# Kernel tuning notes

Hardware: AMD Instinct MI355X
Metric: run time of the kernel (lower is better)

## Reference

```python
import jax, jax.numpy as jnp
import numpy as np

EMBED_DIM = 1024
NUM_HEADS = 16
HEAD_DIM = EMBED_DIM // NUM_HEADS
ROPE_BASE = 10000.0


def rotate_half(x):
    d = x.shape[-1] // 2
    x1, x2 = x[..., :d], x[..., d:]
    return jnp.concatenate((-x2, x1), axis=-1)


def setup_inputs() -> dict:
    key = jax.random.key(0)
    k_x, k_wqkv, k_bqkv, k_wo, k_bo = jax.random.split(key, 5)
    C = EMBED_DIM
    x = jax.random.normal(k_x, (4, 2048, C), dtype=jnp.float32)
    s = 1.0 / np.sqrt(C)
    W_qkv = jax.random.uniform(k_wqkv, (C, 3 * C), minval=-s, maxval=s, dtype=jnp.float32)
    b_qkv = jax.random.uniform(k_bqkv, (3 * C,), minval=-s, maxval=s, dtype=jnp.float32)
    W_out = jax.random.uniform(k_wo, (C, C), minval=-s, maxval=s, dtype=jnp.float32)
    b_out = jax.random.uniform(k_bo, (C,), minval=-s, maxval=s, dtype=jnp.float32)
    return {"x": x, "W_qkv": W_qkv, "b_qkv": b_qkv, "W_out": W_out, "b_out": b_out}


def reference(x, W_qkv, b_qkv, W_out, b_out):
    B, T, C = x.shape
    H, Dh = NUM_HEADS, HEAD_DIM
    # fused QKV projection: [B,T,3C] -> [3,B,H,T,Dh]
    qkv = (x @ W_qkv + b_qkv).reshape(B, T, 3, H, Dh).transpose(2, 0, 3, 1, 4)
    q, k, v = qkv[0], qkv[1], qkv[2]
    # rotary embedding: freqs [T, Dh/2] -> emb [T, Dh]
    inv_freq = 1.0 / (ROPE_BASE ** (jnp.arange(0, Dh, 2, dtype=jnp.float32) / Dh))
    freqs = jnp.arange(T, dtype=jnp.float32)[:, None] * inv_freq[None, :]
    emb = jnp.concatenate((freqs, freqs), axis=-1)  # [T, Dh], broadcasts over B,H
    cos, sin = jnp.cos(emb), jnp.sin(emb)
    q = q * cos + rotate_half(q) * sin
    k = k * cos + rotate_half(k) * sin
    # full (non-causal) attention, manual softmax
    scale = 1.0 / np.sqrt(Dh)
    attn = jax.nn.softmax(jnp.einsum("bhqd,bhkd->bhqk", q, k) * scale, axis=-1)
    out = jnp.einsum("bhqk,bhkd->bhqd", attn, v)  # [B,H,T,Dh]
    out = out.transpose(0, 2, 1, 3).reshape(B, T, C)
    return out @ W_out + b_out
```

## Files before the change

kernel.cpp:

```cpp
#include <hip/hip_runtime.h>
#include <math.h>

#define T_SEQ 2048
#define CDIM  1024
#define NH    16
#define DHD   64
#define BATCH 4
#define MROWS (BATCH * T_SEQ)
#define BHN   (BATCH * NH)

typedef _Float16 f16;
typedef __attribute__((ext_vector_type(8))) _Float16 f16x8;
typedef __attribute__((ext_vector_type(4))) _Float16 f16x4;
typedef __attribute__((ext_vector_type(4))) float f32x4;

__device__ __forceinline__ void gl_lds16(const f16* g, f16* l) {
    __builtin_amdgcn_global_load_lds(
        (const __attribute__((address_space(1))) void*)(g),
        (__attribute__((address_space(3))) void*)(l),
        16, 0, 0);
}

__global__ void rope_tables_kernel(float* __restrict__ ctab, float* __restrict__ stab)
{
    int idx = blockIdx.x * 256 + threadIdx.x;
    int t = idx >> 5, i = idx & 31;
    double inv = pow(10000.0, -(double)(2 * i) / 64.0);
    double a = (double)t * inv;
    ctab[idx] = (float)cos(a);
    stab[idx] = (float)sin(a);
}

__global__ __launch_bounds__(256) void xcvt_kernel(
    const float* __restrict__ X, f16* __restrict__ Xf)
{
    int idx = blockIdx.x * 256 + threadIdx.x;
    const float4* src = (const float4*)X + (size_t)idx * 2;
    float4 a = src[0], b = src[1];
    f16x8 o;
    o[0] = (f16)a.x; o[1] = (f16)a.y; o[2] = (f16)a.z; o[3] = (f16)a.w;
    o[4] = (f16)b.x; o[5] = (f16)b.y; o[6] = (f16)b.z; o[7] = (f16)b.w;
    *((f16x8*)Xf + idx) = o;
}

__global__ __launch_bounds__(64) void wcvt_kernel(
    const float* __restrict__ W, f16* __restrict__ Wt, int N)
{
    int lane = threadIdx.x;
    int k0 = blockIdx.x * 8;
    int n = blockIdx.y * 64 + lane;
    f16x8 o;
#pragma unroll
    for (int j = 0; j < 8; j++) o[j] = (f16)W[(size_t)(k0 + j) * N + n];
    *(f16x8*)(Wt + (size_t)n * CDIM + k0) = o;
}

#define GEMM_MAINLOOP(Aimg, Bimg, M0, N0)                                         \
    __shared__ f16 As[128][32], Bs[128][32];                                      \
    const int tid = threadIdx.x, wave = tid >> 6, lane = tid & 63;                \
    const int l16 = lane & 15, quad = lane >> 4;                                  \
    const int wm = wave >> 1, wn = wave & 1;                                      \
    f32x4 acc[4][4];                                                              \
    _Pragma("unroll") for (int i = 0; i < 4; i++)                                 \
        _Pragma("unroll") for (int j = 0; j < 4; j++)                             \
            acc[i][j] = (f32x4){0.f, 0.f, 0.f, 0.f};                              \
    const f16* sbase = (wave < 2) ? (Aimg) : (Bimg);                              \
    f16* lbase = ((wave < 2) ? &As[0][0] : &Bs[0][0]) + (wave & 1) * 2048;        \
    const size_t srow0 = ((wave < 2) ? (size_t)(M0) : (size_t)(N0)) + (wave & 1) * 64; \
    const int srow = lane >> 2, schunk = (lane & 3) << 3;                         \
    for (int k0 = 0; k0 < CDIM; k0 += 32) {                                       \
        _Pragma("unroll") for (int it = 0; it < 4; it++)                          \
            gl_lds16(sbase + (srow0 + it * 16 + srow) * CDIM + k0 + schunk,       \
                     lbase + it * 512);                                           \
        __syncthreads();                                                          \
        f16x8 fa[4], fb[4];                                                       \
        _Pragma("unroll") for (int mi = 0; mi < 4; mi++)                          \
            fa[mi] = *(const f16x8*)&As[wm * 64 + mi * 16 + l16][quad * 8];       \
        _Pragma("unroll") for (int ni = 0; ni < 4; ni++)                          \
            fb[ni] = *(const f16x8*)&Bs[wn * 64 + ni * 16 + l16][quad * 8];       \
        _Pragma("unroll") for (int mi = 0; mi < 4; mi++)                          \
            _Pragma("unroll") for (int ni = 0; ni < 4; ni++)                      \
                acc[mi][ni] = __builtin_amdgcn_mfma_f32_16x16x32_f16(             \
                    fa[mi], fb[ni], acc[mi][ni], 0, 0, 0);                        \
        __syncthreads();                                                          \
    }

__global__ __launch_bounds__(256) void qkv_gemm_kernel(
    const f16* __restrict__ Xf, const f16* __restrict__ Wt,
    const float* __restrict__ bias,
    const float* __restrict__ ctab, const float* __restrict__ stab,
    f16* __restrict__ qf, f16* __restrict__ kf, f16* __restrict__ vf)
{
    const int m0 = blockIdx.x * 128;
    const int n0 = blockIdx.y * 128;
    GEMM_MAINLOOP(Xf, Wt, m0, n0)

    const int ncol0 = n0 + wn * 64;
    const int w = ncol0 >> 10;
    const int h = (ncol0 >> 6) & 15;
    const int b = m0 >> 11;
    const int trow0 = (m0 & 2047) + wm * 64 + quad * 4;
    float bia[4];
#pragma unroll
    for (int ni = 0; ni < 4; ni++) bia[ni] = bias[ncol0 + ni * 16 + l16];

    if (w < 2) {
        f16* oq = w ? kf : qf;
        const float sc = w ? 1.0f : 0.125f;
#pragma unroll
        for (int mi = 0; mi < 4; mi++) {
#pragma unroll
            for (int i = 0; i < 4; i++) {
                int t = trow0 + mi * 16 + i;
                size_t rowoff = ((size_t)(b * NH + h) * T_SEQ + t) * DHD;
#pragma unroll
                for (int np = 0; np < 2; np++) {
                    int d = np * 16 + l16;
                    float v0 = acc[mi][np][i] + bia[np];
                    float v1 = acc[mi][np + 2][i] + bia[np + 2];
                    float c = ctab[(t << 5) + d];
                    float s = stab[(t << 5) + d];
                    oq[rowoff + d]      = (f16)((v0 * c - v1 * s) * sc);
                    oq[rowoff + d + 32] = (f16)((v1 * c + v0 * s) * sc);
                }
            }
        }
    } else {
#pragma unroll
        for (int mi = 0; mi < 4; mi++) {
#pragma unroll
            for (int i = 0; i < 4; i++) {
                int t = trow0 + mi * 16 + i;
                size_t rowoff = ((size_t)(b * NH + h) * T_SEQ + t) * DHD;
#pragma unroll
                for (int ni = 0; ni < 4; ni++)
                    vf[rowoff + ni * 16 + l16] = (f16)(acc[mi][ni][i] + bia[ni]);
            }
        }
    }
}

__global__ __launch_bounds__(256) void vt_kernel(
    const f16* __restrict__ vf, f16* __restrict__ vt)
{
    __shared__ f16 Ls[64][72];
    const int tid = threadIdx.x;
    const int tb = blockIdx.x;
    const int bh = blockIdx.y;
#pragma unroll
    for (int p = 0; p < 2; p++) {
        int idx = tid + p * 256;
        int r = idx >> 3, c8 = (idx & 7) << 3;
        *(f16x8*)&Ls[r][c8] =
            *(const f16x8*)(vf + ((size_t)bh * T_SEQ + tb * 64 + r) * DHD + c8);
    }
    __syncthreads();
#pragma unroll
    for (int p = 0; p < 2; p++) {
        int idx = tid + p * 256;
        int d = idx >> 3, t8 = (idx & 7) << 3;
        f16x8 o;
#pragma unroll
        for (int j = 0; j < 8; j++) o[j] = Ls[t8 + j][d];
        *(f16x8*)(vt + ((size_t)bh * DHD + d) * T_SEQ + (size_t)tb * 64 + t8) = o;
    }
}

__global__ __launch_bounds__(256, 2) void attn_kernel(
    const f16* __restrict__ qf, const f16* __restrict__ kf,
    const f16* __restrict__ vt, f16* __restrict__ ab)
{
    __shared__ f16 Kb[2][64][72];
    __shared__ f16 Vb[2][64][72];
    __shared__ f16 Pb[4][64][40];
    __shared__ float Lb[4][64];

    const int tid  = threadIdx.x;
    const int wave = tid >> 6, lane = tid & 63;
    const int l16  = lane & 15, quad = lane >> 4;
    const int qt = blockIdx.x;
    const int bh = blockIdx.y;
    const int q0 = qt * 256 + wave * 64;

    const f16* kbase = kf + (size_t)bh * T_SEQ * DHD;
    const f16* vbase = vt + (size_t)bh * DHD * T_SEQ;

    f16x8 qfr[4][2];
#pragma unroll
    for (int qs = 0; qs < 4; qs++) {
        const f16* qrow = qf + ((size_t)bh * T_SEQ + q0 + qs * 16 + l16) * DHD;
        qfr[qs][0] = *(const f16x8*)(qrow + quad * 8);
        qfr[qs][1] = *(const f16x8*)(qrow + 32 + quad * 8);
    }

    f32x4 o[4][4];
#pragma unroll
    for (int qs = 0; qs < 4; qs++)
#pragma unroll
        for (int dt = 0; dt < 4; dt++) o[qs][dt] = (f32x4){0.f, 0.f, 0.f, 0.f};
    float lp[4] = {0.f, 0.f, 0.f, 0.f};

    const int srow = tid >> 3;
    const int scol = (tid & 7) << 3;

    f16x8 kreg[2], vreg[2];
#pragma unroll
    for (int r = 0; r < 2; r++) {
        kreg[r] = *(const f16x8*)(kbase + (size_t)(srow + r * 32) * DHD + scol);
        vreg[r] = *(const f16x8*)(vbase + (size_t)(srow + r * 32) * T_SEQ + scol);
    }
#pragma unroll
    for (int r = 0; r < 2; r++) {
        *(f16x8*)&Kb[0][srow + r * 32][scol] = kreg[r];
        *(f16x8*)&Vb[0][srow + r * 32][scol] = vreg[r];
    }
    __syncthreads();

    for (int kt = 0; kt < 32; kt++) {
        const int buf = kt & 1;
        if (kt < 31) {
#pragma unroll
            for (int r = 0; r < 2; r++) {
                kreg[r] = *(const f16x8*)(kbase + (size_t)((kt + 1) * 64 + srow + r * 32) * DHD + scol);
                vreg[r] = *(const f16x8*)(vbase + (size_t)(srow + r * 32) * T_SEQ + (kt + 1) * 64 + scol);
            }
        }

#pragma unroll
        for (int half = 0; half < 2; half++) {
            f32x4 sc[2][4];
#pragma unroll
            for (int k2 = 0; k2 < 2; k2++)
#pragma unroll
                for (int qs = 0; qs < 4; qs++) sc[k2][qs] = (f32x4){0.f, 0.f, 0.f, 0.f};
#pragma unroll
            for (int k2 = 0; k2 < 2; k2++) {
                const int keyt = half * 2 + k2;
#pragma unroll
                for (int ks = 0; ks < 2; ks++) {
                    f16x8 kfr = *(const f16x8*)&Kb[buf][keyt * 16 + l16][ks * 32 + quad * 8];
#pragma unroll
                    for (int qs = 0; qs < 4; qs++)
                        sc[k2][qs] = __builtin_amdgcn_mfma_f32_16x16x32_f16(
                            kfr, qfr[qs][ks], sc[k2][qs], 0, 0, 0);
                }
            }
#pragma unroll
            for (int k2 = 0; k2 < 2; k2++) {
#pragma unroll
                for (int qs = 0; qs < 4; qs++) {
                    f16x4 pv;
#pragma unroll
                    for (int i = 0; i < 4; i++) {
                        float p = __expf(sc[k2][qs][i]);
                        lp[qs] += p;
                        pv[i] = (f16)p;
                    }
                    *(f16x4*)&Pb[wave][qs * 16 + l16][k2 * 16 + quad * 4] = pv;
                }
            }
            f16x8 pfr[4];
#pragma unroll
            for (int qs = 0; qs < 4; qs++)
                pfr[qs] = *(const f16x8*)&Pb[wave][qs * 16 + l16][quad * 8];
#pragma unroll
            for (int dt = 0; dt < 4; dt++) {
                f16x8 vfr = *(const f16x8*)&Vb[buf][dt * 16 + l16][half * 32 + quad * 8];
#pragma unroll
                for (int qs = 0; qs < 4; qs++)
                    o[qs][dt] = __builtin_amdgcn_mfma_f32_16x16x32_f16(
                        pfr[qs], vfr, o[qs][dt], 0, 0, 0);
            }
        }

        if (kt < 31) {
#pragma unroll
            for (int r = 0; r < 2; r++) {
                *(f16x8*)&Kb[buf ^ 1][srow + r * 32][scol] = kreg[r];
                *(f16x8*)&Vb[buf ^ 1][srow + r * 32][scol] = vreg[r];
            }
        }
        __syncthreads();
    }

#pragma unroll
    for (int qs = 0; qs < 4; qs++) {
        float l = lp[qs];
        l += __shfl_xor(l, 16);
        l += __shfl_xor(l, 32);
        Lb[wave][qs * 16 + l16] = 1.f / l;
    }

    const int b = bh >> 4, h = bh & 15;
#pragma unroll
    for (int qs = 0; qs < 4; qs++) {
        f32x4 iv = *(const f32x4*)&Lb[wave][qs * 16 + quad * 4];
#pragma unroll
        for (int i = 0; i < 4; i++) {
            int m = b * T_SEQ + qt * 256 + wave * 64 + qs * 16 + quad * 4 + i;
#pragma unroll
            for (int dt = 0; dt < 4; dt++)
                ab[(size_t)m * CDIM + h * 64 + dt * 16 + l16] = (f16)(o[qs][dt][i] * iv[i]);
        }
    }
}

__global__ __launch_bounds__(256) void out_gemm_kernel(
    const f16* __restrict__ Ab, const f16* __restrict__ Wt,
    const float* __restrict__ bias, float* __restrict__ out)
{
    const int m0 = blockIdx.x * 128;
    const int n0 = blockIdx.y * 128;
    GEMM_MAINLOOP(Ab, Wt, m0, n0)

    const int ncol0 = n0 + wn * 64;
    float bia[4];
#pragma unroll
    for (int ni = 0; ni < 4; ni++) bia[ni] = bias[ncol0 + ni * 16 + l16];
#pragma unroll
    for (int mi = 0; mi < 4; mi++) {
#pragma unroll
        for (int i = 0; i < 4; i++) {
            int m = m0 + wm * 64 + mi * 16 + quad * 4 + i;
#pragma unroll
            for (int ni = 0; ni < 4; ni++)
                out[(size_t)m * CDIM + ncol0 + ni * 16 + l16] = acc[mi][ni][i] + bia[ni];
        }
    }
}

extern "C" void kernel_launch(void* const* d_in, const int* in_sizes, int n_in,
                              void* d_out, int out_size, void* d_ws, size_t ws_size,
                              hipStream_t stream)
{
    const float* x    = (const float*)d_in[0];
    const float* Wqkv = (const float*)d_in[1];
    const float* bqkv = (const float*)d_in[2];
    const float* Wout = (const float*)d_in[3];
    const float* bout = (const float*)d_in[4];
    float* out = (float*)d_out;

    const size_t XSZ  = (size_t)MROWS * CDIM;
    const size_t WQSZ = (size_t)3072 * CDIM;
    const size_t WOSZ = (size_t)CDIM * CDIM;
    const size_t QSZ  = (size_t)BHN * T_SEQ * DHD;

    char* p = (char*)d_ws;
    f16* Xf  = (f16*)p; p += XSZ * 2;
    f16* Wqt = (f16*)p; p += WQSZ * 2;
    f16* Wot = (f16*)p; p += WOSZ * 2;
    f16* qf  = (f16*)p; p += QSZ * 2;
    f16* kf  = (f16*)p; p += QSZ * 2;
    f16* vf  = (f16*)p; p += QSZ * 2;
    f16* vtb = (f16*)p; p += QSZ * 2;
    f16* ab  = (f16*)p; p += QSZ * 2;
    float* ctab = (float*)p; p += T_SEQ * 32 * 4;
    float* stab = (float*)p; p += T_SEQ * 32 * 4;

    rope_tables_kernel<<<256, 256, 0, stream>>>(ctab, stab);
    xcvt_kernel<<<(int)(XSZ / 8 / 256), 256, 0, stream>>>(x, Xf);
    wcvt_kernel<<<dim3(128, 48), 64, 0, stream>>>(Wqkv, Wqt, 3072);
    wcvt_kernel<<<dim3(128, 16), 64, 0, stream>>>(Wout, Wot, 1024);
    qkv_gemm_kernel<<<dim3(64, 24), 256, 0, stream>>>(
        Xf, Wqt, bqkv, ctab, stab, qf, kf, vf);
    vt_kernel<<<dim3(32, BHN), 256, 0, stream>>>(vf, vtb);
    attn_kernel<<<dim3(8, BHN), 256, 0, stream>>>(qf, kf, vtb, ab);
    out_gemm_kernel<<<dim3(64, 8), 256, 0, stream>>>(ab, Wot, bout, out);
}
```

Baseline: 307.1 us.

## Single-buffer attention LDS, raise occupancy, fold log2e into Q for exp2

```diff
diff --git a/kernel.cpp b/kernel.cpp
--- a/kernel.cpp
+++ b/kernel.cpp
@@ -106,7 +106,7 @@
 
     if (w < 2) {
         f16* oq = w ? kf : qf;
-        const float sc = w ? 1.0f : 0.125f;
+        const float sc = w ? 1.0f : 0.125f * 1.44269504088896f;
 #pragma unroll
         for (int mi = 0; mi < 4; mi++) {
 #pragma unroll
@@ -166,20 +166,21 @@
     }
 }
 
-__global__ __launch_bounds__(256, 2) void attn_kernel(
+__global__ __launch_bounds__(256, 3) void attn_kernel(
     const f16* __restrict__ qf, const f16* __restrict__ kf,
     const f16* __restrict__ vt, f16* __restrict__ ab)
 {
-    __shared__ f16 Kb[2][64][72];
-    __shared__ f16 Vb[2][64][72];
-    __shared__ f16 Pb[4][64][40];
+    __shared__ f16 Kb[64][68];
+    __shared__ f16 Vb[64][68];
+    __shared__ f16 Pb[4][64][36];
     __shared__ float Lb[4][64];
 
     const int tid  = threadIdx.x;
     const int wave = tid >> 6, lane = tid & 63;
     const int l16  = lane & 15, quad = lane >> 4;
-    const int qt = blockIdx.x;
-    const int bh = blockIdx.y;
+    const int bid = blockIdx.x;
+    const int bh = bid & 63;
+    const int qt = bid >> 6;
     const int q0 = qt * 256 + wave * 64;
 
     const f16* kbase = kf + (size_t)bh * T_SEQ * DHD;
@@ -204,27 +205,23 @@
     const int scol = (tid & 7) << 3;
 
     f16x8 kreg[2], vreg[2];
-#pragma unroll
-    for (int r = 0; r < 2; r++) {
-        kreg[r] = *(const f16x8*)(kbase + (size_t)(srow + r * 32) * DHD + scol);
-        vreg[r] = *(const f16x8*)(vbase + (size_t)(srow + r * 32) * T_SEQ + scol);
-    }
-#pragma unroll
-    for (int r = 0; r < 2; r++) {
-        *(f16x8*)&Kb[0][srow + r * 32][scol] = kreg[r];
-        *(f16x8*)&Vb[0][srow + r * 32][scol] = vreg[r];
-    }
+#define PREFETCH(KT)                                                              \
+    _Pragma("unroll") for (int r = 0; r < 2; r++) {                               \
+        kreg[r] = *(const f16x8*)(kbase + (size_t)((KT) * 64 + srow + r * 32) * DHD + scol); \
+        vreg[r] = *(const f16x8*)(vbase + (size_t)(srow + r * 32) * T_SEQ + (KT) * 64 + scol); \
+    }
+#define COMMIT()                                                                  \
+    _Pragma("unroll") for (int r = 0; r < 2; r++) {                               \
+        *(f16x8*)&Kb[srow + r * 32][scol] = kreg[r];                              \
+        *(f16x8*)&Vb[srow + r * 32][scol] = vreg[r];                              \
+    }
+
+    PREFETCH(0)
+    COMMIT()
     __syncthreads();
 
     for (int kt = 0; kt < 32; kt++) {
-        const int buf = kt & 1;
-        if (kt < 31) {
-#pragma unroll
-            for (int r = 0; r < 2; r++) {
-                kreg[r] = *(const f16x8*)(kbase + (size_t)((kt + 1) * 64 + srow + r * 32) * DHD + scol);
-                vreg[r] = *(const f16x8*)(vbase + (size_t)(srow + r * 32) * T_SEQ + (kt + 1) * 64 + scol);
-            }
-        }
+        if (kt < 31) { PREFETCH(kt + 1) }
 
 #pragma unroll
         for (int half = 0; half < 2; half++) {
@@ -238,7 +235,7 @@
                 const int keyt = half * 2 + k2;
 #pragma unroll
                 for (int ks = 0; ks < 2; ks++) {
-                    f16x8 kfr = *(const f16x8*)&Kb[buf][keyt * 16 + l16][ks * 32 + quad * 8];
+                    f16x8 kfr = *(const f16x8*)&Kb[keyt * 16 + l16][ks * 32 + quad * 8];
 #pragma unroll
                     for (int qs = 0; qs < 4; qs++)
                         sc[k2][qs] = __builtin_amdgcn_mfma_f32_16x16x32_f16(
@@ -249,13 +246,14 @@
             for (int k2 = 0; k2 < 2; k2++) {
 #pragma unroll
                 for (int qs = 0; qs < 4; qs++) {
+                    float p0 = exp2f(sc[k2][qs][0]);
+                    float p1 = exp2f(sc[k2][qs][1]);
+                    float p2 = exp2f(sc[k2][qs][2]);
+                    float p3 = exp2f(sc[k2][qs][3]);
+                    lp[qs] += (p0 + p1) + (p2 + p3);
                     f16x4 pv;
-#pragma unroll
-                    for (int i = 0; i < 4; i++) {
-                        float p = __expf(sc[k2][qs][i]);
-                        lp[qs] += p;
-                        pv[i] = (f16)p;
-                    }
+                    pv[0] = (f16)p0; pv[1] = (f16)p1;
+                    pv[2] = (f16)p2; pv[3] = (f16)p3;
                     *(f16x4*)&Pb[wave][qs * 16 + l16][k2 * 16 + quad * 4] = pv;
                 }
             }
@@ -265,7 +263,7 @@
                 pfr[qs] = *(const f16x8*)&Pb[wave][qs * 16 + l16][quad * 8];
 #pragma unroll
             for (int dt = 0; dt < 4; dt++) {
-                f16x8 vfr = *(const f16x8*)&Vb[buf][dt * 16 + l16][half * 32 + quad * 8];
+                f16x8 vfr = *(const f16x8*)&Vb[dt * 16 + l16][half * 32 + quad * 8];
 #pragma unroll
                 for (int qs = 0; qs < 4; qs++)
                     o[qs][dt] = __builtin_amdgcn_mfma_f32_16x16x32_f16(
@@ -273,15 +271,12 @@
             }
         }
 
-        if (kt < 31) {
-#pragma unroll
-            for (int r = 0; r < 2; r++) {
-                *(f16x8*)&Kb[buf ^ 1][srow + r * 32][scol] = kreg[r];
-                *(f16x8*)&Vb[buf ^ 1][srow + r * 32][scol] = vreg[r];
-            }
-        }
         __syncthreads();
-    }
+        if (kt < 31) { COMMIT() }
+        __syncthreads();
+    }
+#undef PREFETCH
+#undef COMMIT
 
 #pragma unroll
     for (int qs = 0; qs < 4; qs++) {
@@ -364,6 +359,6 @@
     qkv_gemm_kernel<<<dim3(64, 24), 256, 0, stream>>>(
         Xf, Wqt, bqkv, ctab, stab, qf, kf, vf);
     vt_kernel<<<dim3(32, BHN), 256, 0, stream>>>(vf, vtb);
-    attn_kernel<<<dim3(8, BHN), 256, 0, stream>>>(qf, kf, vtb, ab);
+    attn_kernel<<<512, 256, 0, stream>>>(qf, kf, vtb, ab);
     out_gemm_kernel<<<dim3(64, 8), 256, 0, stream>>>(ab, Wot, bout, out);
 }
```

New measurement: 478.0 us. +55.6%, slower.
